# Kernel tuning notes

Hardware: AMD Instinct MI355X
Metric: run time of the kernel (lower is better)

## Reference

```python
import jax, jax.numpy as jnp
import numpy as np

CELLS = 56
EPS = 1e-9

def setup_inputs() -> dict:
    key = jax.random.key(0)
    k1, k2 = jax.random.split(key)
    B = 512
    F = CELLS * CELLS * 15  # 47040 floats per sample
    output = jax.random.uniform(k1, (B, F), dtype=jnp.float32)
    target = jax.random.uniform(k2, (B, F), dtype=jnp.float32)
    return {"output": output, "target": target}

def reference(output, target):
    B = output.shape[0]
    # reshape flat vector into [B, cells^2, 15] slots: x,y,w,h,conf,classes[5:14]
    o = output.reshape(B, CELLS * CELLS, 15)
    t = target.reshape(B, CELLS * CELLS, 15)
    # coordinate loss: only x (slice [i*15 : i*15+1]) plus sqrt(w)/sqrt(h) terms
    coord = (o[..., 0] - t[..., 0]) ** 2 \
          + (jnp.sqrt(o[..., 2]) - jnp.sqrt(t[..., 2])) ** 2 \
          + (jnp.sqrt(o[..., 3]) - jnp.sqrt(t[..., 3])) ** 2
    # binary cross-entropy on confidence (slot 4)
    conf = -(t[..., 4] * jnp.log(o[..., 4] + EPS)
             + (1.0 - t[..., 4]) * jnp.log(1.0 - o[..., 4] + EPS))
    # class loss: sum of squared diffs over slots 5:14 (9 elements)
    cls = jnp.sum((t[..., 5:14] - o[..., 5:14]) ** 2, axis=-1)
    # cell is counted only if output x-coordinate is nonzero (torch.is_nonzero gate)
    mask = o[..., 0] != 0
    per_cell = jnp.where(mask, coord + conf + cls, 0.0)
    return jnp.sum(per_cell)
```

## Files before the change

kernel.cpp:

```cpp
#include <hip/hip_runtime.h>


#define EPSF 1e-9f
#define LN2F 0.69314718055994530942f

#define GRID    1792
#define KITERS  7
#define BLK_E   (KITERS * 1920)
#define FAST_N  (GRID * BLK_E)

typedef float f32x4 __attribute__((ext_vector_type(4)));

__device__ __forceinline__ float bce_of(float ox, float tx) {
    const float l1 = __log2f(ox + EPSF);
    const float l2 = __log2f((1.f - ox) + EPSF);
    return -LN2F * (tx * l1 + (1.f - tx) * l2);
}

__global__ __launch_bounds__(256, 7) void yolo_loss_wave(
    const float* __restrict__ o, const float* __restrict__ t,
    float* __restrict__ out_sum)
{
    const int tid  = threadIdx.x;
    const int lane = tid & 63;
    const int wv   = tid >> 6;
    const bool act = lane < 60;

    const f32x4* o4 = (const f32x4*)o;
    const f32x4* t4 = (const f32x4*)t;

    const unsigned le  = 4u * (unsigned)lane;
    const unsigned c0r = le / 15u;
    const unsigned c3r = (le + 3u) / 15u;
    const unsigned s0  = le - c0r * 15u;
    const int d_lo = (int)((15u * c0r) >> 2);
    const int d_hi = (int)((15u * c3r) >> 2);
    const unsigned j_own = (le + 14u) / 15u;
    const unsigned gpos  = 15u * j_own - le;
    const bool gsel1 = (gpos & 1u) != 0u;
    const bool gsel2 = (gpos & 2u) != 0u;

    bool is4[4], ksq[4], kz[4], wr[4];
    #pragma unroll
    for (int j = 0; j < 4; ++j) {
        const unsigned s = s0 + (unsigned)j;
        is4[j] = (s == 4u);
        ksq[j] = (s == 2u) | (s == 3u) | (s == 17u);
        kz [j] = (s == 1u) | (s == 14u) | (s == 16u);
        wr [j] = (s >= 15u);
    }

    auto window_sum = [&](f32x4 ov, f32x4 tv) -> float {
        const float gA   = gsel1 ? ov.y : ov.x;
        const float gB   = gsel1 ? ov.w : ov.z;
        const float gown = gsel2 ? gB : gA;
        const float glo  = __shfl(gown, d_lo, 64);
        const float ghi  = __shfl(gown, d_hi, 64);

        const float oe[4] = {ov.x, ov.y, ov.z, ov.w};
        const float te[4] = {tv.x, tv.y, tv.z, tv.w};

        float oc = oe[3], tc = te[3];
        #pragma unroll
        for (int j = 2; j >= 0; --j) { oc = is4[j] ? oe[j] : oc; tc = is4[j] ? te[j] : tc; }
        const float bce = bce_of(oc, tc);

        float sum = 0.f;
        #pragma unroll
        for (int j = 0; j < 4; ++j) {
            const float gate = wr[j] ? ghi : glo;
            const float ox = oe[j], tx = te[j];
            const float d  = ox - tx;
            const float sq = d * d;
            const float s23 = (ox + tx) - 2.f * __builtin_amdgcn_sqrtf(ox * tx);
            float c = ksq[j] ? s23 : sq;
            c = is4[j] ? bce : c;
            c = kz[j] ? 0.f : c;
            c = (gate != 0.f) ? c : 0.f;
            sum += c;
        }
        return sum;
    };

    const unsigned blk_f4 = blockIdx.x * (unsigned)(BLK_E / 4);
    float acc = 0.f;
    #pragma unroll 1
    for (int k = 0; k < KITERS; ++k) {
        const unsigned wbase = blk_f4 + (unsigned)k * 480u + (unsigned)wv * 120u;
        f32x4 ovA = {0.f,0.f,0.f,0.f}, tvA = {0.f,0.f,0.f,0.f};
        f32x4 ovB = {0.f,0.f,0.f,0.f}, tvB = {0.f,0.f,0.f,0.f};
        if (act) {
            ovA = o4[wbase + (unsigned)lane];
            tvA = t4[wbase + (unsigned)lane];
            ovB = o4[wbase + 60u + (unsigned)lane];
            tvB = t4[wbase + 60u + (unsigned)lane];
        }
        const float sA = window_sum(ovA, tvA);
        const float sB = window_sum(ovB, tvB);
        acc += act ? (sA + sB) : 0.f;
    }

    #pragma unroll
    for (int off = 32; off; off >>= 1) acc += __shfl_down(acc, off, 64);
    __shared__ float wsum[4];
    if ((tid & 63) == 0) wsum[tid >> 6] = acc;
    __syncthreads();
    if (tid == 0) atomicAdd(out_sum, wsum[0] + wsum[1] + wsum[2] + wsum[3]);
}

__global__ __launch_bounds__(256) void yolo_loss_generic(
    const float* __restrict__ o, const float* __restrict__ t,
    float* __restrict__ out_sum, int n4, int n)
{
    const int tid = threadIdx.x;
    const int stride = gridDim.x * 256;
    const float4* o4 = (const float4*)o;
    const float4* t4 = (const float4*)t;
    float acc = 0.f;

    for (int i = blockIdx.x * 256 + tid; i < n4; i += stride) {
        const float4 ov = o4[i];
        const float4 tv = t4[i];
        const unsigned e0 = (unsigned)i * 4u;
        const unsigned c0 = e0 / 15u;
        const unsigned c3 = (e0 + 3u) / 15u;
        const unsigned s0 = e0 - c0 * 15u;
        const float glo = o[c0 * 15u], ghi = o[c3 * 15u];
        const float oe[4] = {ov.x, ov.y, ov.z, ov.w};
        const float te[4] = {tv.x, tv.y, tv.z, tv.w};
        #pragma unroll
        for (int j = 0; j < 4; ++j) {
            unsigned s = s0 + (unsigned)j;
            const bool wrap = s >= 15u;
            s = wrap ? s - 15u : s;
            const float gate = wrap ? ghi : glo;
            const float ox = oe[j], tx = te[j];
            const float d = ox - tx;
            const float sq = d * d;
            const float s23 = (ox + tx) - 2.f * __builtin_amdgcn_sqrtf(ox * tx);
            float c = ((s == 2u) | (s == 3u)) ? s23 : sq;
            c = (s == 4u) ? bce_of(ox, tx) : c;
            c = ((s == 1u) | (s == 14u)) ? 0.f : c;
            c = (gate != 0.f) ? c : 0.f;
            acc += c;
        }
    }
    const int tail0 = n4 * 4;
    if (blockIdx.x == 0 && tid < n - tail0) {
        const unsigned e = (unsigned)(tail0 + tid);
        const unsigned cell = e / 15u;
        const unsigned s = e - cell * 15u;
        const float gate = o[cell * 15u];
        const float ox = o[e], tx = t[e];
        const float d = ox - tx;
        float c = d * d;
        c = ((s == 2u) | (s == 3u)) ? (ox + tx) - 2.f * __builtin_amdgcn_sqrtf(ox * tx) : c;
        c = (s == 4u) ? bce_of(ox, tx) : c;
        c = ((s == 1u) | (s == 14u)) ? 0.f : c;
        c = (gate != 0.f) ? c : 0.f;
        acc += c;
    }
    #pragma unroll
    for (int off = 32; off; off >>= 1) acc += __shfl_down(acc, off, 64);
    __shared__ float wsum[4];
    if ((tid & 63) == 0) wsum[tid >> 6] = acc;
    __syncthreads();
    if (tid == 0) atomicAdd(out_sum, wsum[0] + wsum[1] + wsum[2] + wsum[3]);
}

extern "C" void kernel_launch(void* const* d_in, const int* in_sizes, int n_in,
                              void* d_out, int out_size, void* d_ws, size_t ws_size,
                              hipStream_t stream) {
    const float* o = (const float*)d_in[0];
    const float* t = (const float*)d_in[1];
    float* out = (float*)d_out;
    const int n = in_sizes[0];

    hipMemsetAsync(out, 0, sizeof(float), stream);

    if (n == FAST_N) {
        yolo_loss_wave<<<GRID, 256, 0, stream>>>(o, t, out);
    } else {
        yolo_loss_generic<<<2940, 256, 0, stream>>>(o, t, out, n / 4, n);
    }
}
```

Before: 208.4 us.

## Stream inputs through LDS with async global_load_lds in a 4-slot pipeline

Replaces the register loads with direct global-to-LDS async loads (global_load_lds) into a 4-slot ring buffer per wave, keeping three stages in flight via explicit vmcnt waits. Gate values are read from LDS instead of cross-lane shuffles. The goal is deeper memory-level parallelism on a bandwidth-bound reduction. In exchange it uses LDS capacity, drops the occupancy hint, and depends on hand-written waitcnt ordering.

```diff
diff --git a/kernel.cpp b/kernel.cpp
--- a/kernel.cpp
+++ b/kernel.cpp
@@ -5,8 +5,8 @@
 #define LN2F 0.69314718055994530942f
 
 #define GRID    1792
-#define KITERS  7
-#define BLK_E   (KITERS * 1920)
+#define NSTAGE  14
+#define BLK_E   (NSTAGE * 960)
 #define FAST_N  (GRID * BLK_E)
 
 typedef float f32x4 __attribute__((ext_vector_type(4)));
@@ -17,10 +17,14 @@
     return -LN2F * (tx * l1 + (1.f - tx) * l2);
 }
 
-__global__ __launch_bounds__(256, 7) void yolo_loss_wave(
+__global__ __launch_bounds__(256) void yolo_loss_alds(
     const float* __restrict__ o, const float* __restrict__ t,
     float* __restrict__ out_sum)
 {
+    __shared__ f32x4 obuf[4][4][64];
+    __shared__ f32x4 tbuf[4][4][64];
+    __shared__ float wsum[4];
+
     const int tid  = threadIdx.x;
     const int lane = tid & 63;
     const int wv   = tid >> 6;
@@ -33,12 +37,8 @@
     const unsigned c0r = le / 15u;
     const unsigned c3r = (le + 3u) / 15u;
     const unsigned s0  = le - c0r * 15u;
-    const int d_lo = (int)((15u * c0r) >> 2);
-    const int d_hi = (int)((15u * c3r) >> 2);
-    const unsigned j_own = (le + 14u) / 15u;
-    const unsigned gpos  = 15u * j_own - le;
-    const bool gsel1 = (gpos & 1u) != 0u;
-    const bool gsel2 = (gpos & 2u) != 0u;
+    const unsigned glo_off = c0r * 15u;
+    const unsigned ghi_off = c3r * 15u;
 
     bool is4[4], ksq[4], kz[4], wr[4];
     #pragma unroll
@@ -50,12 +50,26 @@
         wr [j] = (s >= 15u);
     }
 
-    auto window_sum = [&](f32x4 ov, f32x4 tv) -> float {
-        const float gA   = gsel1 ? ov.y : ov.x;
-        const float gB   = gsel1 ? ov.w : ov.z;
-        const float gown = gsel2 ? gB : gA;
-        const float glo  = __shfl(gown, d_lo, 64);
-        const float ghi  = __shfl(gown, d_hi, 64);
+    const unsigned wv_f4 = blockIdx.x * (unsigned)(BLK_E / 4) + (unsigned)wv * 60u;
+
+    auto issue = [&](int kk) {
+        const int slot = kk & 3;
+        if (act) {
+            const unsigned g = wv_f4 + (unsigned)kk * 240u + (unsigned)lane;
+            __builtin_amdgcn_global_load_lds((const void*)(o4 + g),
+                                             (void*)&obuf[slot][wv][0], 16, 0, 0);
+            __builtin_amdgcn_global_load_lds((const void*)(t4 + g),
+                                             (void*)&tbuf[slot][wv][0], 16, 0, 0);
+        }
+    };
+
+    auto consume = [&](int kk) -> float {
+        const int slot = kk & 3;
+        const f32x4 ov = obuf[slot][wv][lane];
+        const f32x4 tv = tbuf[slot][wv][lane];
+        const float* owin = (const float*)&obuf[slot][wv][0];
+        const float glo = owin[glo_off];
+        const float ghi = owin[ghi_off];
 
         const float oe[4] = {ov.x, ov.y, ov.z, ov.w};
         const float te[4] = {tv.x, tv.y, tv.z, tv.w};
@@ -79,31 +93,32 @@
             c = (gate != 0.f) ? c : 0.f;
             sum += c;
         }
-        return sum;
+        return act ? sum : 0.f;
     };
 
-    const unsigned blk_f4 = blockIdx.x * (unsigned)(BLK_E / 4);
+    issue(0); issue(1); issue(2);
+
     float acc = 0.f;
     #pragma unroll 1
-    for (int k = 0; k < KITERS; ++k) {
-        const unsigned wbase = blk_f4 + (unsigned)k * 480u + (unsigned)wv * 120u;
-        f32x4 ovA = {0.f,0.f,0.f,0.f}, tvA = {0.f,0.f,0.f,0.f};
-        f32x4 ovB = {0.f,0.f,0.f,0.f}, tvB = {0.f,0.f,0.f,0.f};
-        if (act) {
-            ovA = o4[wbase + (unsigned)lane];
-            tvA = t4[wbase + (unsigned)lane];
-            ovB = o4[wbase + 60u + (unsigned)lane];
-            tvB = t4[wbase + 60u + (unsigned)lane];
-        }
-        const float sA = window_sum(ovA, tvA);
-        const float sB = window_sum(ovB, tvB);
-        acc += act ? (sA + sB) : 0.f;
-    }
+    for (int k = 0; k < NSTAGE - 3; ++k) {
+        issue(k + 3);
+        asm volatile("s_waitcnt vmcnt(6)" ::: "memory");
+        __builtin_amdgcn_sched_barrier(0);
+        acc += consume(k);
+    }
+    asm volatile("s_waitcnt vmcnt(4)" ::: "memory");
+    __builtin_amdgcn_sched_barrier(0);
+    acc += consume(NSTAGE - 3);
+    asm volatile("s_waitcnt vmcnt(2)" ::: "memory");
+    __builtin_amdgcn_sched_barrier(0);
+    acc += consume(NSTAGE - 2);
+    asm volatile("s_waitcnt vmcnt(0)" ::: "memory");
+    __builtin_amdgcn_sched_barrier(0);
+    acc += consume(NSTAGE - 1);
 
     #pragma unroll
     for (int off = 32; off; off >>= 1) acc += __shfl_down(acc, off, 64);
-    __shared__ float wsum[4];
-    if ((tid & 63) == 0) wsum[tid >> 6] = acc;
+    if (lane == 0) wsum[wv] = acc;
     __syncthreads();
     if (tid == 0) atomicAdd(out_sum, wsum[0] + wsum[1] + wsum[2] + wsum[3]);
 }
@@ -179,7 +194,7 @@
     hipMemsetAsync(out, 0, sizeof(float), stream);
 
     if (n == FAST_N) {
-        yolo_loss_wave<<<GRID, 256, 0, stream>>>(o, t, out);
+        yolo_loss_alds<<<GRID, 256, 0, stream>>>(o, t, out);
     } else {
         yolo_loss_generic<<<2940, 256, 0, stream>>>(o, t, out, n / 4, n);
     }
```

Result: no change. 205.0 us (-1.7%).
